# Optimization experiments

Hardware: AMD Instinct MI355X
Metric: run time of the kernel (lower is better)

Reference implementation:

```python
import jax, jax.numpy as jnp
import numpy as np

B, T, E = 2, 2048, 2048
H, NOPE, ROPE, VD, KVR, DR = 16, 64, 32, 64, 256, 2
QKD = NOPE + ROPE  # 96
LOWR = KVR // 4    # hypernet low_rank=4 -> 64


def _rope_angles(position, dim):
    # freqs_cis angles: pos * 10000^(-2i/dim), matching torch rotary with theta=10000
    inv = jnp.exp(jnp.arange(0, dim, 2, dtype=jnp.float32) * (-jnp.log(jnp.float32(10000.0)) / dim))
    return position.astype(jnp.float32)[..., None] * inv  # (1, T, dim//2)


def _apply_rotary(x, ang):
    # x: (B,T,H,D); pairs are consecutive elements (view_as_complex semantics)
    x2 = x.reshape(x.shape[:-1] + (-1, 2))
    c = jnp.cos(ang)[:, :, None, :]
    s = jnp.sin(ang)[:, :, None, :]
    xr, xi = x2[..., 0], x2[..., 1]
    return jnp.stack([xr * c - xi * s, xr * s + xi * c], axis=-1).reshape(x.shape)


def _layernorm(x, g, b, eps=1e-5):
    m = jnp.mean(x, axis=-1, keepdims=True)
    v = jnp.var(x, axis=-1, keepdims=True)
    return (x - m) * jax.lax.rsqrt(v + eps) * g + b


def _sinusoid_pe(t, d):
    pos = jnp.arange(t, dtype=jnp.float32)[:, None]
    div = jnp.exp(jnp.arange(0, d, 2, dtype=jnp.float32) * (-jnp.log(jnp.float32(10000.0)) / d))
    pe = jnp.zeros((t, d), dtype=jnp.float32)
    pe = pe.at[:, 0::2].set(jnp.sin(pos * div)).at[:, 1::2].set(jnp.cos(pos * div))
    return pe


def setup_inputs() -> dict:
    key = jax.random.key(0)
    ks = jax.random.split(key, 16)
    sd = 0.02
    return {
        "query": jax.random.normal(ks[0], (B, T, E), jnp.float32),
        "key": jax.random.normal(ks[1], (B, T, E), jnp.float32),
        "value": jax.random.normal(ks[2], (B, T, E), jnp.float32),
        "position": jnp.arange(T, dtype=jnp.int32)[None, :],
        # weights stored transposed for right-multiply (x @ W)
        "wq": jax.random.normal(ks[3], (E, H * QKD), jnp.float32) * sd,
        "wkv_a": jax.random.normal(ks[4], (E, KVR + ROPE), jnp.float32) * sd,
        "kv_gamma": jnp.ones((KVR,), jnp.float32),
        "kv_beta": jnp.zeros((KVR,), jnp.float32),
        # torch layout (H*(NOPE+VD), KVR) kept for faithful view(H,-1,KVR) absorb
        "wkv_b": jax.random.normal(ks[5], (H * (NOPE + VD), KVR), jnp.float32) * sd,
        "wo": jax.random.normal(ks[6], (H * VD, E), jnp.float32) * sd,
        "fc_c_w": jax.random.normal(ks[7], (KVR, LOWR), jnp.float32) * sd,
        "fc_c_b": jnp.zeros((LOWR,), jnp.float32),
        "fc_p_w": jax.random.normal(ks[8], (KVR, LOWR), jnp.float32) * sd,
        "fc_p_b": jnp.zeros((LOWR,), jnp.float32),
    }


def reference(query, key, value, position, wq, wkv_a, kv_gamma, kv_beta, wkv_b, wo,
              fc_c_w, fc_c_b, fc_p_w, fc_p_b):
    bsz, seqlen, _ = query.shape
    # queries: low-rank-free path (q_lora_rank=0)
    q = (query @ wq).reshape(bsz, seqlen, H, QKD)
    q_nope, q_pe = q[..., :NOPE], q[..., NOPE:]
    ang = _rope_angles(position, ROPE)  # (1, T, ROPE//2)
    q_pe = _apply_rotary(q_pe, ang[:, -seqlen:])
    # key/value latent projection
    kv_all = key @ wkv_a  # (B, T, KVR+ROPE)
    kv, k_pe = kv_all[..., :KVR], kv_all[..., KVR:]
    k_pe = _apply_rotary(k_pe[:, :, None, :], ang)[:, :, 0, :]  # (B, T, ROPE)
    kv_norm = _layernorm(kv, kv_gamma, kv_beta)  # (B, T, KVR)
    # hypernetwork temporal downsampling weights (train path, T_input=kv_norm)
    t = -(-seqlen // DR)
    C = jnp.repeat(_sinusoid_pe(t, KVR), DR, axis=0)[:seqlen]  # (T, KVR)
    C2 = C @ fc_c_w + fc_c_b           # (T, LOWR)
    P2 = kv_norm @ fc_p_w + fc_p_b     # (B, T, LOWR)
    W = jax.nn.sigmoid(jnp.einsum('tc,bsc->bts', C2, P2))  # (B, T, T)
    idx = jnp.arange(seqlen)
    chunk = idx // DR
    # chunk mask: cumulative within-chunk causal accumulation
    zero_mask = ((chunk[:, None] == chunk[None, :]) & (idx[None, :] <= idx[:, None])).astype(query.dtype)
    kv_t = jnp.einsum('bts,bsc->btc', W * zero_mask, kv_norm)  # (B, T, KVR)
    # stride-aware causal mask: attend completed chunk-end slots + own in-progress slot
    allowed = (idx[None, :] == idx[:, None]) | ((idx[None, :] < idx[:, None]) & (((idx[None, :] + 1) % DR) == 0))
    attn_mask = jnp.where(allowed, jnp.float32(0.0), jnp.float32(-1e30))
    # absorbed MLA attention
    wb = wkv_b.reshape(H, NOPE + VD, KVR)
    q_abs = jnp.einsum('bshd,hdc->bshc', q_nope, wb[:, :NOPE])  # (B, S, H, KVR)
    scores = (jnp.einsum('bshc,btc->bsht', q_abs, kv_t)
              + jnp.einsum('bshr,btr->bsht', q_pe, k_pe)) * (QKD ** -0.5)
    scores = scores + attn_mask[None, :, None, :]
    attn = jax.nn.softmax(scores, axis=-1)
    x = jnp.einsum('bsht,btc->bshc', attn, kv_t)
    x = jnp.einsum('bshc,hdc->bshd', x, wb[:, NOPE:])  # (B, S, H, VD)
    return x.reshape(bsz, seqlen, H * VD) @ wo
```

## Files before the change

kernel.cpp:

```cpp
#include <hip/hip_runtime.h>
#include <stddef.h>

typedef unsigned short u16;
typedef unsigned short u16x8 __attribute__((ext_vector_type(8)));
typedef short s16x8 __attribute__((ext_vector_type(8)));
typedef float f32x4 __attribute__((ext_vector_type(4)));

#define B_ 2
#define T_ 2048
#define E_ 2048
#define H_ 16

__device__ inline float us2f(u16 u){
  unsigned int i = ((unsigned int)u) << 16;
  return __builtin_bit_cast(float, i);
}
__device__ inline u16 f2us(float f){
  unsigned int x = __builtin_bit_cast(unsigned int, f);
  unsigned int r = (x + 0x7fffu + ((x >> 16) & 1u)) >> 16;
  return (u16)r;
}
__device__ inline f32x4 mfma32(s16x8 a, s16x8 b, f32x4 c){
  return __builtin_amdgcn_mfma_f32_16x16x32_bf16(a, b, c, 0, 0, 0);
}
__device__ inline s16x8 ld8(const u16* p){
  return __builtin_bit_cast(s16x8, *(const u16x8*)p);
}
__device__ inline void gload_lds16(const u16* g, u16* l){
  __builtin_amdgcn_global_load_lds(
      (const __attribute__((address_space(1))) unsigned int*)(g),
      (__attribute__((address_space(3))) unsigned int*)(l), 16, 0, 0);
}

__global__ __launch_bounds__(256) void prep_weights(
    const float* __restrict__ wq, const float* __restrict__ wkva,
    const float* __restrict__ wo, const float* __restrict__ wkvb,
    u16* __restrict__ wqT, u16* __restrict__ wkvaT, u16* __restrict__ woT,
    u16* __restrict__ wkvbB)
{
  __shared__ float tile[32][33];
  const int bid = blockIdx.x;
  const int tid = threadIdx.x;
  if (bid < 5696) {
    const float* in; u16* out; int R, C, bx, by;
    if (bid < 3072)      { in = wq;   out = wqT;   R = 2048; C = 1536; bx = bid % 48;          by = bid / 48; }
    else if (bid < 3648) { in = wkva; out = wkvaT; R = 2048; C = 288;  bx = (bid-3072) % 9;    by = (bid-3072) / 9; }
    else                 { in = wo;   out = woT;   R = 1024; C = 2048; bx = (bid-3648) % 64;   by = (bid-3648) / 64; }
    int tx = tid & 31, ty = tid >> 5;
    int c0 = bx * 32, r0 = by * 32;
    for (int i = ty; i < 32; i += 8){
      int r = r0 + i, c = c0 + tx;
      tile[i][tx] = (r < R && c < C) ? in[(size_t)r * C + c] : 0.f;
    }
    __syncthreads();
    for (int i = ty; i < 32; i += 8){
      int c = c0 + i, r = r0 + tx;
      if (c < C && r < R) out[(size_t)c * R + r] = f2us(tile[tx][i]);
    }
  } else {
    int i = (bid - 5696) * 1024 + tid * 4;
    f32x4 v = *(const f32x4*)(wkvb + i);
    wkvbB[i]   = f2us(v[0]); wkvbB[i+1] = f2us(v[1]);
    wkvbB[i+2] = f2us(v[2]); wkvbB[i+3] = f2us(v[3]);
  }
}

__global__ __launch_bounds__(256) void cvt2_f32_bf16(const float* __restrict__ a,
    const float* __restrict__ b, u16* __restrict__ oa, u16* __restrict__ ob, int n_each)
{
  int idx = (blockIdx.x * 256 + threadIdx.x) * 4;
  const float* in; u16* out; int i;
  if (idx < n_each){ in = a; out = oa; i = idx; }
  else             { in = b; out = ob; i = idx - n_each; }
  if (i + 3 < n_each){
    f32x4 v = *(const f32x4*)(in + i);
    out[i]   = f2us(v[0]); out[i+1] = f2us(v[1]);
    out[i+2] = f2us(v[2]); out[i+3] = f2us(v[3]);
  }
}

template<int A_F32, int OUT_F32>
__global__ __launch_bounds__(256) void gemm_bt(const void* __restrict__ Ap,
    const u16* __restrict__ Bt, void* __restrict__ Cp, int M, int N, int K)
{
  __shared__ __align__(16) u16 As[64][40];
  __shared__ __align__(16) u16 Bs[64][40];
  const int tid  = threadIdx.x;
  const int lane = tid & 63;
  const int wid  = tid >> 6;
  const int quad = lane >> 4;
  const int col  = lane & 15;
  const int bm = blockIdx.y * 64;
  const int bn = blockIdx.x * 64;
  const int lr = tid >> 2;
  const int lc = (tid & 3) * 8;
  const int waveM = wid >> 1, waveN = wid & 1;

  f32x4 acc[2][2];
  for (int i = 0; i < 2; ++i)
    for (int j = 0; j < 2; ++j)
      acc[i][j] = (f32x4){0.f, 0.f, 0.f, 0.f};

  const u16x8 zero8 = {0,0,0,0,0,0,0,0};
  const bool bok = (bn + lr) < N;
  const u16*   arow16 = (const u16*)Ap   + (size_t)(bm + lr) * K + lc;
  const float* arow32 = (const float*)Ap + (size_t)(bm + lr) * K + lc;
  const u16* brow = Bt + (size_t)(bn + lr) * K + lc;

  for (int kk = 0; kk < K; kk += 32) {
    u16x8 av;
    if (A_F32) {
      f32x4 a0 = *(const f32x4*)(arow32 + kk);
      f32x4 a1 = *(const f32x4*)(arow32 + kk + 4);
      av[0]=f2us(a0[0]); av[1]=f2us(a0[1]); av[2]=f2us(a0[2]); av[3]=f2us(a0[3]);
      av[4]=f2us(a1[0]); av[5]=f2us(a1[1]); av[6]=f2us(a1[2]); av[7]=f2us(a1[3]);
    } else {
      av = *(const u16x8*)(arow16 + kk);
    }
    u16x8 bv = bok ? *(const u16x8*)(brow + kk) : zero8;
    __syncthreads();
    *(u16x8*)&As[lr][lc] = av;
    *(u16x8*)&Bs[lr][lc] = bv;
    __syncthreads();
    s16x8 af0 = ld8(&As[waveM*32 + col][quad*8]);
    s16x8 af1 = ld8(&As[waveM*32 + 16 + col][quad*8]);
    s16x8 bf0 = ld8(&Bs[waveN*32 + col][quad*8]);
    s16x8 bf1 = ld8(&Bs[waveN*32 + 16 + col][quad*8]);
    acc[0][0] = mfma32(af0, bf0, acc[0][0]);
    acc[0][1] = mfma32(af0, bf1, acc[0][1]);
    acc[1][0] = mfma32(af1, bf0, acc[1][0]);
    acc[1][1] = mfma32(af1, bf1, acc[1][1]);
  }
  for (int am = 0; am < 2; ++am)
    for (int bnn = 0; bnn < 2; ++bnn)
      for (int i = 0; i < 4; ++i) {
        int r = bm + waveM*32 + am*16 + quad*4 + i;
        int c = bn + waveN*32 + bnn*16 + col;
        if (c < N){
          if (OUT_F32) ((float*)Cp)[(size_t)r * N + c] = acc[am][bnn][i];
          else         ((u16*)Cp)[(size_t)r * N + c]   = f2us(acc[am][bnn][i]);
        }
      }
}

template<int OUT_F32>
__global__ __launch_bounds__(256) void gemm128(const u16* __restrict__ A,
    const u16* __restrict__ Bt, void* __restrict__ Cp, int M, int N, int K)
{
  __shared__ __align__(16) u16 As[128 * 32];
  __shared__ __align__(16) u16 Bs[128 * 32];
  const int tid  = threadIdx.x;
  const int lane = tid & 63;
  const int wid  = tid >> 6;
  const int quad = lane >> 4;
  const int col  = lane & 15;
  const int bm = blockIdx.y * 128;
  const int bn = blockIdx.x * 128;
  const int waveM = wid >> 1, waveN = wid & 1;

  const int srow = wid * 16 + (lane >> 2);
  const int scol = (lane & 3) * 8;
  const u16* ga = A  + (size_t)(bm + srow) * K + scol;
  const u16* gb = Bt + (size_t)(bn + srow) * K + scol;
  const size_t rowskip = (size_t)64 * K;
  u16* lAs0 = &As[wid * 512];
  u16* lAs1 = &As[wid * 512 + 2048];
  u16* lBs0 = &Bs[wid * 512];
  u16* lBs1 = &Bs[wid * 512 + 2048];

  f32x4 acc[4][4] = {};

  for (int kk = 0; kk < K; kk += 32) {
    __syncthreads();
    gload_lds16(ga + kk,           lAs0);
    gload_lds16(ga + rowskip + kk, lAs1);
    gload_lds16(gb + kk,           lBs0);
    gload_lds16(gb + rowskip + kk, lBs1);
    __syncthreads();
    s16x8 af[4], bf[4];
#pragma unroll
    for (int i = 0; i < 4; ++i) af[i] = ld8(&As[(waveM*64 + i*16 + col) * 32 + quad*8]);
#pragma unroll
    for (int i = 0; i < 4; ++i) bf[i] = ld8(&Bs[(waveN*64 + i*16 + col) * 32 + quad*8]);
#pragma unroll
    for (int i = 0; i < 4; ++i)
#pragma unroll
      for (int j = 0; j < 4; ++j)
        acc[i][j] = mfma32(af[i], bf[j], acc[i][j]);
  }
#pragma unroll
  for (int i = 0; i < 4; ++i)
#pragma unroll
    for (int j = 0; j < 4; ++j)
#pragma unroll
      for (int r = 0; r < 4; ++r) {
        int row = bm + waveM*64 + i*16 + quad*4 + r;
        int c   = bn + waveN*64 + j*16 + col;
        if (OUT_F32) ((float*)Cp)[(size_t)row * N + c] = acc[i][j][r];
        else         ((u16*)Cp)[(size_t)row * N + c]   = f2us(acc[i][j][r]);
      }
}

__global__ __launch_bounds__(256) void gemm128_sk(const u16* __restrict__ A,
    const u16* __restrict__ Bt, u16* __restrict__ Cp0, u16* __restrict__ Cp1,
    int M, int N, int K, int Klen)
{
  __shared__ __align__(16) u16 As[128 * 32];
  __shared__ __align__(16) u16 Bs[128 * 32];
  const int tid  = threadIdx.x;
  const int lane = tid & 63;
  const int wid  = tid >> 6;
  const int quad = lane >> 4;
  const int col  = lane & 15;
  const int bm = blockIdx.y * 128;
  const int bn = blockIdx.x * 128;
  const int kh = blockIdx.z;
  const int waveM = wid >> 1, waveN = wid & 1;

  const int srow = wid * 16 + (lane >> 2);
  const int scol = (lane & 3) * 8;
  const u16* ga = A  + (size_t)(bm + srow) * K + kh * Klen + scol;
  const u16* gb = Bt + (size_t)(bn + srow) * K + kh * Klen + scol;
  const size_t rowskip = (size_t)64 * K;
  u16* lAs0 = &As[wid * 512];
  u16* lAs1 = &As[wid * 512 + 2048];
  u16* lBs0 = &Bs[wid * 512];
  u16* lBs1 = &Bs[wid * 512 + 2048];
  u16* Cp = kh ? Cp1 : Cp0;

  f32x4 acc[4][4] = {};

  for (int kk = 0; kk < Klen; kk += 32) {
    __syncthreads();
    gload_lds16(ga + kk,           lAs0);
    gload_lds16(ga + rowskip + kk, lAs1);
    gload_lds16(gb + kk,           lBs0);
    gload_lds16(gb + rowskip + kk, lBs1);
    __syncthreads();
    s16x8 af[4], bf[4];
#pragma unroll
    for (int i = 0; i < 4; ++i) af[i] = ld8(&As[(waveM*64 + i*16 + col) * 32 + quad*8]);
#pragma unroll
    for (int i = 0; i < 4; ++i) bf[i] = ld8(&Bs[(waveN*64 + i*16 + col) * 32 + quad*8]);
#pragma unroll
    for (int i = 0; i < 4; ++i)
#pragma unroll
      for (int j = 0; j < 4; ++j)
        acc[i][j] = mfma32(af[i], bf[j], acc[i][j]);
  }
#pragma unroll
  for (int i = 0; i < 4; ++i)
#pragma unroll
    for (int j = 0; j < 4; ++j)
#pragma unroll
      for (int r = 0; r < 4; ++r) {
        int row = bm + waveM*64 + i*16 + quad*4 + r;
        int c   = bn + waveN*64 + j*16 + col;
        Cp[(size_t)row * N + c] = f2us(acc[i][j][r]);
      }
}

__global__ __launch_bounds__(256) void qsplit(const u16* __restrict__ qp0,
    const u16* __restrict__ qp1, const int* __restrict__ pos, u16* __restrict__ qh)
{
  int idx = blockIdx.x * 256 + threadIdx.x;
  if (idx >= B_*T_*H_*12) return;
  int c    = idx % 12;
  int rest = idx / 12;
  int h    = rest & 15;
  int row  = rest >> 4;
  int t    = row & (T_ - 1);
  int b    = row >> 11;
  size_t off = (size_t)row * 1536 + h * 96 + c * 8;
  u16x8 v0 = *(const u16x8*)(qp0 + off);
  u16x8 v1 = *(const u16x8*)(qp1 + off);
  u16x8 v;
  if (c < 8) {
#pragma unroll
    for (int k = 0; k < 8; ++k) v[k] = f2us(us2f(v0[k]) + us2f(v1[k]));
  } else {
    int i0 = (c - 8) * 4;
    float pp = (float)pos[t];
#pragma unroll
    for (int k = 0; k < 4; ++k){
      int i = i0 + k;
      float ang = pp * __expf((float)(2*i) * -0.28782313657f);
      float cs = __cosf(ang), sn = __sinf(ang);
      float xr = us2f(v0[2*k])   + us2f(v1[2*k]);
      float xi = us2f(v0[2*k+1]) + us2f(v1[2*k+1]);
      v[2*k]   = f2us(xr * cs - xi * sn);
      v[2*k+1] = f2us(xr * sn + xi * cs);
    }
  }
  u16* dst = qh + ((size_t)(b * 16 + h) * T_ + t) * 96;
  *(u16x8*)(dst + c * 8) = v;
}

__global__ __launch_bounds__(256) void ln_p2_rope(
    const u16* __restrict__ kvall, const float* __restrict__ gamma,
    const float* __restrict__ beta, const float* __restrict__ fcpw,
    const float* __restrict__ fcpb, const int* __restrict__ pos,
    u16* __restrict__ kvn, float* __restrict__ P2, u16* __restrict__ kpe)
{
  const int row = blockIdx.x;
  if (row >= B_ * T_) return;
  const int tid = threadIdx.x;
  const int lane = tid & 63, wid = tid >> 6;
  __shared__ float kvs[256];
  __shared__ float part[256];
  __shared__ float redS[4], redS2[4];
  const u16* src = kvall + (size_t)row * 288;
  float v = us2f(src[tid]);
  float s1 = v, s2 = v * v;
  for (int off = 1; off < 64; off <<= 1){
    s1 += __shfl_xor(s1, off);
    s2 += __shfl_xor(s2, off);
  }
  if (lane == 0){ redS[wid] = s1; redS2[wid] = s2; }
  __syncthreads();
  float S  = redS[0] + redS[1] + redS[2] + redS[3];
  float Q  = redS2[0] + redS2[1] + redS2[2] + redS2[3];
  float mean = S * (1.f / 256.f);
  float var  = Q * (1.f / 256.f) - mean * mean;
  float rstd = rsqrtf(var + 1e-5f);
  float xn = (v - mean) * rstd * gamma[tid] + beta[tid];
  kvs[tid] = xn;
  kvn[(size_t)row * 256 + tid] = f2us(xn);
  __syncthreads();
  {
    int oc = tid & 63, pp = tid >> 6;
    float acc = 0.f;
#pragma unroll 8
    for (int c = pp * 64; c < pp * 64 + 64; ++c)
      acc += kvs[c] * fcpw[c * 64 + oc];
    part[tid] = acc;
  }
  __syncthreads();
  if (tid < 64) {
    P2[(size_t)row * 64 + tid] = fcpb[tid] + part[tid] + part[64 + tid]
                               + part[128 + tid] + part[192 + tid];
  } else if (tid < 80) {
    int i = tid - 64;
    int t = row & (T_ - 1);
    float ang = (float)pos[t] * __expf((float)(2*i) * -0.28782313657f);
    float c = __cosf(ang), s = __sinf(ang);
    float xr = us2f(src[256 + 2*i]);
    float xi = us2f(src[257 + 2*i]);
    kpe[(size_t)row * 32 + 2*i]     = f2us(xr * c - xi * s);
    kpe[(size_t)row * 32 + 2*i + 1] = f2us(xr * s + xi * c);
  }
}

__global__ __launch_bounds__(256) void c2_kernel(const float* __restrict__ fccw,
    const float* __restrict__ fccb, float* __restrict__ C2)
{
  const int t = blockIdx.x, tid = threadIdx.x;
  __shared__ float pe[256];
  __shared__ float part[256];
  float p = (float)(t >> 1);
  if (tid < 128){
    float div = __expf((float)(2*tid) * -0.03597789207f);
    float a = p * div;
    pe[2*tid]   = __sinf(a);
    pe[2*tid+1] = __cosf(a);
  }
  __syncthreads();
  {
    int oc = tid & 63, pp = tid >> 6;
    float acc = 0.f;
#pragma unroll 8
    for (int c = pp * 64; c < pp * 64 + 64; ++c)
      acc += pe[c] * fccw[c * 64 + oc];
    part[tid] = acc;
  }
  __syncthreads();
  if (tid < 64)
    C2[t * 64 + tid] = fccb[tid] + part[tid] + part[64 + tid]
                     + part[128 + tid] + part[192 + tid];
}

__global__ __launch_bounds__(64) void kvt_kernel(const float* __restrict__ C2,
    const float* __restrict__ P2, const u16* __restrict__ kvn, u16* __restrict__ kvt)
{
  const int row = blockIdx.x;
  if (row >= B_ * T_) return;
  const int lane = threadIdx.x;
  const int t = row & (T_ - 1);
  float c2v = C2[t * 64 + lane];
  float da = c2v * P2[(size_t)row * 64 + lane];
  for (int off = 1; off < 64; off <<= 1) da += __shfl_xor(da, off);
  float wtt = 1.f / (1.f + __expf(-da));
  const bool odd = (t & 1);
  float wts = 0.f;
  if (odd){
    float db = c2v * P2[(size_t)(row - 1) * 64 + lane];
    for (int off = 1; off < 64; off <<= 1) db += __shfl_xor(db, off);
    wts = 1.f / (1.f + __expf(-db));
  }
  for (int c = lane; c < 256; c += 64){
    float val = wtt * us2f(kvn[(size_t)row * 256 + c]);
    if (odd) val += wts * us2f(kvn[(size_t)(row - 1) * 256 + c]);
    kvt[(size_t)row * 256 + c] = f2us(val);
  }
}

__global__ __launch_bounds__(256) void vtkc_kernel(const u16* __restrict__ kvb,
    const u16* __restrict__ kpe, u16* __restrict__ Vt, u16* __restrict__ Kc)
{
  __shared__ __align__(16) u16 tile[64][72];
  const int tid = threadIdx.x;
  if (blockIdx.x < 512) {
    const int bid = blockIdx.x;
    const int jt = bid & 15;
    const int h  = (bid >> 4) & 15;
    const int b  = bid >> 8;
    const int jl = tid >> 2;
    const int dseg = (tid & 3) * 16;
    const int j0 = jt * 64;
    {
      int s_ = 2 * (j0 + jl) + 1;
      const u16* src = kvb + ((size_t)(b * T_ + s_)) * 2048 + h * 128 + 64 + dseg;
      *(u16x8*)&tile[jl][dseg]     = *(const u16x8*)(src);
      *(u16x8*)&tile[jl][dseg + 8] = *(const u16x8*)(src + 8);
    }
    __syncthreads();
    const int dl = tid >> 2;
    const int jseg = (tid & 3) * 16;
    u16* dst = Vt + ((size_t)(b * 16 + h) * 64 + dl) * 1024 + j0 + jseg;
    u16x8 o;
    for (int r = 0; r < 8; ++r) o[r] = tile[jseg + r][dl];
    *(u16x8*)dst = o;
    for (int r = 0; r < 8; ++r) o[r] = tile[jseg + 8 + r][dl];
    *(u16x8*)(dst + 8) = o;
  } else {
    int idx = (blockIdx.x - 512) * 256 + tid;
    int c  = idx % 12;
    int j  = (idx / 12) & 1023;
    int bh = idx / (12 * 1024);
    if (bh >= B_ * H_) return;
    int b = bh >> 4, h = bh & 15;
    int t = 2 * j + 1;
    u16x8 v;
    if (c < 8) v = *(const u16x8*)(kvb + ((size_t)(b * T_ + t)) * 2048 + h * 128 + c * 8);
    else       v = *(const u16x8*)(kpe + ((size_t)(b * T_ + t)) * 32 + (c - 8) * 8);
    int kl = j & 63;
    int cs = (c & 12) | ((c & 3) ^ ((kl >> 1) & 3));
    *(u16x8*)(Kc + ((size_t)bh * 1024 + j) * 96 + cs * 8) = v;
  }
}

__global__ __launch_bounds__(256) void attn_kernel(
    const u16* __restrict__ qh, const u16* __restrict__ kvb,
    const u16* __restrict__ kpe, const u16* __restrict__ Kc,
    const u16* __restrict__ Vt, u16* __restrict__ xout)
{
  __shared__ __align__(16) u16 Ks[64 * 96];
  __shared__ __align__(16) u16 Vs[64][72];
  __shared__ __align__(16) u16 pbufA[4][16 * 72];
  const int tid  = threadIdx.x;
  const int wid  = tid >> 6;
  const int lane = tid & 63;
  const int quad = lane >> 4;
  const int col  = lane & 15;
  const int qt   = 31 - (blockIdx.x >> 5);
  const int bh   = blockIdx.x & 31;
  const int b    = bh >> 4;
  const int h    = bh & 15;
  u16* pbuf = pbufA[wid];
  const float scale = 0.10206207262f;
  const u16* KcH = Kc + (size_t)bh * 1024 * 96;
  const u16* VtH = Vt + (size_t)bh * 64 * 1024;
  const int t0 = qt * 64 + wid * 16;
  const int qo = (quad * 8) ^ (((col >> 1) & 3) << 3);

  s16x8 aq0, aq1, aq2;
  {
    const u16* qrow = qh + ((size_t)bh * T_ + t0 + col) * 96;
    aq0 = ld8(qrow + quad * 8);
    aq1 = ld8(qrow + 32 + quad * 8);
    aq2 = ld8(qrow + 64 + quad * 8);
  }
  float sself;
  {
    const int t = t0 + col;
    const u16* qrow = qh + ((size_t)bh * T_ + t) * 96;
    const u16* ka = kvb + ((size_t)(b * T_ + t)) * 2048 + h * 128;
    const u16* kp = kpe + ((size_t)(b * T_ + t)) * 32;
    float a = 0.f;
#pragma unroll
    for (int c = 0; c < 8; ++c){
      u16x8 qv = *(const u16x8*)(qrow + c * 8);
      u16x8 kv = *(const u16x8*)(ka + c * 8);
#pragma unroll
      for (int jj = 0; jj < 8; ++jj) a += us2f(qv[jj]) * us2f(kv[jj]);
    }
#pragma unroll
    for (int c = 0; c < 4; ++c){
      u16x8 qv = *(const u16x8*)(qrow + 64 + c * 8);
      u16x8 kv = *(const u16x8*)(kp + c * 8);
#pragma unroll
      for (int jj = 0; jj < 8; ++jj) a += us2f(qv[jj]) * us2f(kv[jj]);
    }
    sself = a * scale;
  }
  float es[4], lacc[4];
  f32x4 O[4];
#pragma unroll
  for (int i = 0; i < 4; ++i){
    es[i] = __expf(__shfl(sself, quad * 4 + i));
    lacc[i] = 0.f;
  }
#pragma unroll
  for (int nt = 0; nt < 4; ++nt)
#pragma unroll
    for (int i = 0; i < 4; ++i){
      int t = t0 + quad * 4 + i;
      O[nt][i] = es[i] * us2f(kvb[((size_t)(b * T_ + t)) * 2048 + h * 128 + 64 + nt * 16 + col]);
    }

  const int nb = (qt * 32 + 94) >> 6;
  for (int blk = 0; blk < nb; ++blk) {
    const int jb = blk * 64;
    __syncthreads();
    {
      const u16* gk = KcH + (size_t)jb * 96 + (wid * 3) * 512 + lane * 8;
      u16* lk = &Ks[(wid * 3) * 512];
#pragma unroll
      for (int k = 0; k < 3; ++k)
        gload_lds16(gk + k * 512, lk + k * 512);
      int d = tid >> 2, c4 = tid & 3;
      const u16* gv = VtH + (size_t)d * 1024 + jb + c4 * 16;
      u16* lv = &Vs[d][c4 * 16];
      *(u16x8*)(lv)     = *(const u16x8*)(gv);
      *(u16x8*)(lv + 8) = *(const u16x8*)(gv + 8);
    }
    __syncthreads();
#pragma unroll
    for (int cc = 0; cc < 2; ++cc){
      const u16* k0 = &Ks[(cc * 32 + col) * 96];
      const u16* k1 = k0 + 16 * 96;
      f32x4 s0 = {0,0,0,0}, s1 = {0,0,0,0};
      s0 = mfma32(aq0, ld8(k0 + qo), s0);
      s0 = mfma32(aq1, ld8(k0 + 32 + qo), s0);
      s0 = mfma32(aq2, ld8(k0 + 64 + qo), s0);
      s1 = mfma32(aq0, ld8(k1 + qo), s1);
      s1 = mfma32(aq1, ld8(k1 + 32 + qo), s1);
      s1 = mfma32(aq2, ld8(k1 + 64 + qo), s1);
      int key0 = jb + cc * 32 + col;
#pragma unroll
      for (int i = 0; i < 4; ++i){
        int lim = (t0 + quad * 4 + i) >> 1;
        float p0 = (key0 < lim)      ? __expf(s0[i] * scale) : 0.f;
        float p1 = (key0 + 16 < lim) ? __expf(s1[i] * scale) : 0.f;
        lacc[i] += p0 + p1;
        pbuf[(quad * 4 + i) * 72 + cc * 32 + col]      = f2us(p0);
        pbuf[(quad * 4 + i) * 72 + cc * 32 + 16 + col] = f2us(p1);
      }
    }
    asm volatile("s_waitcnt lgkmcnt(0)" ::: "memory");
    __builtin_amdgcn_sched_barrier(0);
#pragma unroll
    for (int cc = 0; cc < 2; ++cc){
      s16x8 pf = ld8(&pbuf[col * 72 + cc * 32 + quad * 8]);
#pragma unroll
      for (int nt = 0; nt < 4; ++nt)
        O[nt] = mfma32(pf, ld8(&Vs[nt * 16 + col][cc * 32 + quad * 8]), O[nt]);
    }
  }
#pragma unroll
  for (int i = 0; i < 4; ++i){
    float l = lacc[i];
    l += __shfl_xor(l, 1);
    l += __shfl_xor(l, 2);
    l += __shfl_xor(l, 4);
    l += __shfl_xor(l, 8);
    lacc[i] = es[i] + l;
  }
#pragma unroll
  for (int nt = 0; nt < 4; ++nt)
#pragma unroll
    for (int i = 0; i < 4; ++i){
      int t = t0 + quad * 4 + i;
      xout[((size_t)(b * T_ + t)) * 1024 + h * 64 + nt * 16 + col] = f2us(O[nt][i] / lacc[i]);
    }
}

extern "C" void kernel_launch(void* const* d_in, const int* in_sizes, int n_in,
                              void* d_out, int out_size, void* d_ws, size_t ws_size,
                              hipStream_t stream)
{
  (void)in_sizes; (void)n_in; (void)out_size; (void)ws_size;
  const float* query = (const float*)d_in[0];
  const float* key_  = (const float*)d_in[1];
  const int*   pos   = (const int*)d_in[3];
  const float* wq    = (const float*)d_in[4];
  const float* wkva  = (const float*)d_in[5];
  const float* gamma = (const float*)d_in[6];
  const float* beta  = (const float*)d_in[7];
  const float* wkvb  = (const float*)d_in[8];
  const float* wo    = (const float*)d_in[9];
  const float* fccw  = (const float*)d_in[10];
  const float* fccb  = (const float*)d_in[11];
  const float* fcpw  = (const float*)d_in[12];
  const float* fcpb  = (const float*)d_in[13];

  char* p = (char*)d_ws;
  auto alloc = [&](size_t bytes) -> void* {
    void* r = (void*)p;
    p += (bytes + 255) & ~(size_t)255;
    return r;
  };
  u16* wqT    = (u16*)alloc(1536ull * 2048 * 2);
  u16* wkvaT  = (u16*)alloc(288ull  * 2048 * 2);
  u16* woT    = (u16*)alloc(2048ull * 1024 * 2);
  u16* wkvbB  = (u16*)alloc(2048ull * 256 * 2);
  u16* queryB = (u16*)alloc(4096ull * 2048 * 2);
  u16* keyB   = (u16*)alloc(4096ull * 2048 * 2);
  u16* qp0    = (u16*)alloc(4096ull * 1536 * 2);
  u16* qp1    = (u16*)alloc(4096ull * 1536 * 2);
  u16* qh     = (u16*)alloc(65536ull * 96 * 2);
  u16* kvall  = (u16*)alloc(4096ull * 288 * 2);
  u16* kvn    = (u16*)alloc(4096ull * 256 * 2);
  u16* kpe    = (u16*)alloc(4096ull * 32 * 2);
  float* P2   = (float*)alloc(4096ull * 64 * 4);
  float* C2   = (float*)alloc(2048ull * 64 * 4);
  u16* kvt    = (u16*)alloc(4096ull * 256 * 2);
  u16* kvb    = (u16*)alloc(4096ull * 2048 * 2);
  u16* Kc     = (u16*)alloc(32ull * 1024 * 96 * 2);
  u16* Vt     = (u16*)alloc(2048ull * 1024 * 2);
  u16* x      = (u16*)alloc(4096ull * 1024 * 2);

  prep_weights<<<6208, 256, 0, stream>>>(wq, wkva, wo, wkvb, wqT, wkvaT, woT, wkvbB);
  cvt2_f32_bf16<<<16384, 256, 0, stream>>>(query, key_, queryB, keyB, 4096 * 2048);

  gemm128_sk<<<dim3(12, 32, 2), 256, 0, stream>>>(queryB, wqT, qp0, qp1, 4096, 1536, 2048, 1024);
  gemm_bt<0,0><<<dim3(5, 64), 256, 0, stream>>>(keyB, wkvaT, kvall, 4096, 288, 2048);

  qsplit<<<3072, 256, 0, stream>>>(qp0, qp1, pos, qh);
  ln_p2_rope<<<4096, 256, 0, stream>>>(kvall, gamma, beta, fcpw, fcpb, pos, kvn, P2, kpe);
  c2_kernel<<<2048, 256, 0, stream>>>(fccw, fccb, C2);
  kvt_kernel<<<4096, 64, 0, stream>>>(C2, P2, kvn, kvt);

  gemm128<0><<<dim3(16, 32), 256, 0, stream>>>(kvt, wkvbB, kvb, 4096, 2048, 256);
  vtkc_kernel<<<2048, 256, 0, stream>>>(kvb, kpe, Vt, Kc);
  attn_kernel<<<1024, 256, 0, stream>>>(qh, kvb, kpe, Kc, Vt, x);

  gemm128<1><<<dim3(16, 32), 256, 0, stream>>>(x, woT, d_out, 4096, 2048, 1024);
}
```

Before: 352.3 us.

## Split Q projection K four ways and XCD-swizzle GEMM block mapping

The Q projection GEMM now splits K into four slices instead of two, giving 1536 blocks that write four partial products. qsplit sums all four before applying rotary. The 128x128 GEMMs use a 1D grid with a stride-8 swizzle, so that consecutive blocks sent to the same XCD cover neighbouring tiles and share L2. Kc, Vt and x now alias the larger partial-product buffer to save workspace, at the cost of more partial-sum traffic and more bf16 rounding steps in the Q projection.

Result: no change. 358.4 us (+1.7%).

```diff
diff --git a/kernel.cpp b/kernel.cpp
--- a/kernel.cpp
+++ b/kernel.cpp
@@ -145,17 +145,22 @@
 
 template<int OUT_F32>
 __global__ __launch_bounds__(256) void gemm128(const u16* __restrict__ A,
-    const u16* __restrict__ Bt, void* __restrict__ Cp, int M, int N, int K)
+    const u16* __restrict__ Bt, void* __restrict__ Cp, int M, int N, int K, int gx)
 {
   __shared__ __align__(16) u16 As[128 * 32];
   __shared__ __align__(16) u16 Bs[128 * 32];
+  const int lin = blockIdx.x;
+  const int cpx = gridDim.x >> 3;
+  const int swz = (lin & 7) * cpx + (lin >> 3);
+  const int bxi = swz % gx;
+  const int byi = swz / gx;
   const int tid  = threadIdx.x;
   const int lane = tid & 63;
   const int wid  = tid >> 6;
   const int quad = lane >> 4;
   const int col  = lane & 15;
-  const int bm = blockIdx.y * 128;
-  const int bn = blockIdx.x * 128;
+  const int bm = byi * 128;
+  const int bn = bxi * 128;
   const int waveM = wid >> 1, waveN = wid & 1;
 
   const int srow = wid * 16 + (lane >> 2);
@@ -201,20 +206,25 @@
       }
 }
 
-__global__ __launch_bounds__(256) void gemm128_sk(const u16* __restrict__ A,
-    const u16* __restrict__ Bt, u16* __restrict__ Cp0, u16* __restrict__ Cp1,
+__global__ __launch_bounds__(256) void gemm128_sk4(const u16* __restrict__ A,
+    const u16* __restrict__ Bt, u16* __restrict__ qp,
     int M, int N, int K, int Klen)
 {
   __shared__ __align__(16) u16 As[128 * 32];
   __shared__ __align__(16) u16 Bs[128 * 32];
+  const int lin = blockIdx.x;
+  const int swz = (lin & 7) * 192 + (lin >> 3);
+  const int kh  = swz / 384;
+  const int rem = swz % 384;
+  const int byi = rem / 12;
+  const int bxi = rem % 12;
   const int tid  = threadIdx.x;
   const int lane = tid & 63;
   const int wid  = tid >> 6;
   const int quad = lane >> 4;
   const int col  = lane & 15;
-  const int bm = blockIdx.y * 128;
-  const int bn = blockIdx.x * 128;
-  const int kh = blockIdx.z;
+  const int bm = byi * 128;
+  const int bn = bxi * 128;
   const int waveM = wid >> 1, waveN = wid & 1;
 
   const int srow = wid * 16 + (lane >> 2);
@@ -226,7 +236,7 @@
   u16* lAs1 = &As[wid * 512 + 2048];
   u16* lBs0 = &Bs[wid * 512];
   u16* lBs1 = &Bs[wid * 512 + 2048];
-  u16* Cp = kh ? Cp1 : Cp0;
+  u16* Cp = qp + (size_t)kh * M * N;
 
   f32x4 acc[4][4] = {};
 
@@ -260,9 +270,10 @@
       }
 }
 
-__global__ __launch_bounds__(256) void qsplit(const u16* __restrict__ qp0,
-    const u16* __restrict__ qp1, const int* __restrict__ pos, u16* __restrict__ qh)
-{
+__global__ __launch_bounds__(256) void qsplit(const u16* __restrict__ qp,
+    const int* __restrict__ pos, u16* __restrict__ qh)
+{
+  const size_t PS = 4096ull * 1536;
   int idx = blockIdx.x * 256 + threadIdx.x;
   if (idx >= B_*T_*H_*12) return;
   int c    = idx % 12;
@@ -272,12 +283,15 @@
   int t    = row & (T_ - 1);
   int b    = row >> 11;
   size_t off = (size_t)row * 1536 + h * 96 + c * 8;
-  u16x8 v0 = *(const u16x8*)(qp0 + off);
-  u16x8 v1 = *(const u16x8*)(qp1 + off);
+  u16x8 v0 = *(const u16x8*)(qp + off);
+  u16x8 v1 = *(const u16x8*)(qp + PS + off);
+  u16x8 v2 = *(const u16x8*)(qp + 2*PS + off);
+  u16x8 v3 = *(const u16x8*)(qp + 3*PS + off);
   u16x8 v;
   if (c < 8) {
 #pragma unroll
-    for (int k = 0; k < 8; ++k) v[k] = f2us(us2f(v0[k]) + us2f(v1[k]));
+    for (int k = 0; k < 8; ++k)
+      v[k] = f2us((us2f(v0[k]) + us2f(v1[k])) + (us2f(v2[k]) + us2f(v3[k])));
   } else {
     int i0 = (c - 8) * 4;
     float pp = (float)pos[t];
@@ -286,8 +300,8 @@
       int i = i0 + k;
       float ang = pp * __expf((float)(2*i) * -0.28782313657f);
       float cs = __cosf(ang), sn = __sinf(ang);
-      float xr = us2f(v0[2*k])   + us2f(v1[2*k]);
-      float xi = us2f(v0[2*k+1]) + us2f(v1[2*k+1]);
+      float xr = (us2f(v0[2*k])   + us2f(v1[2*k]))   + (us2f(v2[2*k])   + us2f(v3[2*k]));
+      float xi = (us2f(v0[2*k+1]) + us2f(v1[2*k+1])) + (us2f(v2[2*k+1]) + us2f(v3[2*k+1]));
       v[2*k]   = f2us(xr * cs - xi * sn);
       v[2*k+1] = f2us(xr * sn + xi * cs);
     }
@@ -616,8 +630,7 @@
   u16* wkvbB  = (u16*)alloc(2048ull * 256 * 2);
   u16* queryB = (u16*)alloc(4096ull * 2048 * 2);
   u16* keyB   = (u16*)alloc(4096ull * 2048 * 2);
-  u16* qp0    = (u16*)alloc(4096ull * 1536 * 2);
-  u16* qp1    = (u16*)alloc(4096ull * 1536 * 2);
+  u16* qp     = (u16*)alloc(4ull * 4096 * 1536 * 2);
   u16* qh     = (u16*)alloc(65536ull * 96 * 2);
   u16* kvall  = (u16*)alloc(4096ull * 288 * 2);
   u16* kvn    = (u16*)alloc(4096ull * 256 * 2);
@@ -626,24 +639,26 @@
   float* C2   = (float*)alloc(2048ull * 64 * 4);
   u16* kvt    = (u16*)alloc(4096ull * 256 * 2);
   u16* kvb    = (u16*)alloc(4096ull * 2048 * 2);
-  u16* Kc     = (u16*)alloc(32ull * 1024 * 96 * 2);
-  u16* Vt     = (u16*)alloc(2048ull * 1024 * 2);
-  u16* x      = (u16*)alloc(4096ull * 1024 * 2);
+  char* q8 = (char*)qp;
+  u16* Kc = (u16*)q8;
+  u16* Vt = (u16*)(q8 + ((32ull*1024*96*2 + 255) & ~255ull));
+  u16* x  = (u16*)(q8 + ((32ull*1024*96*2 + 255) & ~255ull)
+                      + ((2048ull*1024*2   + 255) & ~255ull));
 
   prep_weights<<<6208, 256, 0, stream>>>(wq, wkva, wo, wkvb, wqT, wkvaT, woT, wkvbB);
   cvt2_f32_bf16<<<16384, 256, 0, stream>>>(query, key_, queryB, keyB, 4096 * 2048);
 
-  gemm128_sk<<<dim3(12, 32, 2), 256, 0, stream>>>(queryB, wqT, qp0, qp1, 4096, 1536, 2048, 1024);
+  gemm128_sk4<<<1536, 256, 0, stream>>>(queryB, wqT, qp, 4096, 1536, 2048, 512);
   gemm_bt<0,0><<<dim3(5, 64), 256, 0, stream>>>(keyB, wkvaT, kvall, 4096, 288, 2048);
 
-  qsplit<<<3072, 256, 0, stream>>>(qp0, qp1, pos, qh);
+  qsplit<<<3072, 256, 0, stream>>>(qp, pos, qh);
   ln_p2_rope<<<4096, 256, 0, stream>>>(kvall, gamma, beta, fcpw, fcpb, pos, kvn, P2, kpe);
   c2_kernel<<<2048, 256, 0, stream>>>(fccw, fccb, C2);
   kvt_kernel<<<4096, 64, 0, stream>>>(C2, P2, kvn, kvt);
 
-  gemm128<0><<<dim3(16, 32), 256, 0, stream>>>(kvt, wkvbB, kvb, 4096, 2048, 256);
+  gemm128<0><<<512, 256, 0, stream>>>(kvt, wkvbB, kvb, 4096, 2048, 256, 16);
   vtkc_kernel<<<2048, 256, 0, stream>>>(kvb, kpe, Vt, Kc);
   attn_kernel<<<1024, 256, 0, stream>>>(qh, kvb, kpe, Kc, Vt, x);
 
-  gemm128<1><<<dim3(16, 32), 256, 0, stream>>>(x, woT, d_out, 4096, 2048, 1024);
-}
+  gemm128<1><<<512, 256, 0, stream>>>(x, woT, d_out, 4096, 2048, 1024, 16);
+}
```
